# Optimization experiments

Hardware: AMD Instinct MI355X
Metric: run time of the kernel (lower is better)

Reference implementation:

```python
import jax, jax.numpy as jnp
import numpy as np

NUM_DIRECTIONS = 64
NUM_STEPS = 64
D = 64
NEG_INF = -1e9  # matches the original's -inf sentinel of 1e9


def _sample_directions(n):
    # Mirrors WeightedEulerCurve._obtainDirection with np.random.seed(4)
    np.random.seed(4)
    out = []
    for _ in range(n):
        phi = np.random.uniform(0, np.pi * 2)
        costheta = np.random.uniform(-1, 1)
        theta = np.arccos(costheta)
        out.append([np.sin(theta) * np.cos(phi), np.sin(theta) * np.sin(phi), np.cos(theta)])
    return np.asarray(out, dtype=np.float32)


def setup_inputs() -> dict:
    key = jax.random.key(0)
    # strictly positive -> dense cubical complex (every voxel is a vertex,
    # every adjacent pair an edge, etc.), matching torch.nonzero on x>0
    x = jax.random.uniform(key, (D, D, D), dtype=jnp.float32) + 1e-3
    dirs = jnp.asarray(_sample_directions(NUM_DIRECTIONS))  # (K, 3)
    return {"x": x, "dirs": dirs}


def _pairmax(a, axis):
    n = a.shape[axis]
    return jnp.maximum(jax.lax.slice_in_dim(a, 0, n - 1, axis=axis),
                       jax.lax.slice_in_dim(a, 1, n, axis=axis))


def _curve_contrib(heights, vals, intervals):
    # heights: (K, N) per-direction simplex heights; vals: (N,) shared weights
    K = heights.shape[0]
    idx = jnp.argsort(heights, axis=-1)
    sorted_h = jnp.take_along_axis(heights, idx, axis=-1)
    sorted_v = jnp.take(vals, idx)                                    # (K, N)
    csum = jnp.concatenate([jnp.zeros((K, 1), heights.dtype),
                            jnp.cumsum(sorted_v, axis=-1)], axis=-1)  # (K, N+1)
    padded_h = jnp.concatenate([jnp.full((K, 1), NEG_INF, heights.dtype),
                                sorted_h], axis=-1)                   # (K, N+1)
    ptr = jax.vmap(lambda h: jnp.searchsorted(h, intervals, side='right'))(padded_h) - 1
    return jnp.take_along_axis(csum, ptr, axis=-1)                    # (K, num_intervals)


def _wect(x, dirs, num_steps):
    d = x.shape[0]
    K = dirs.shape[0]
    r = jnp.arange(d, dtype=x.dtype)
    d0, d1, d2 = dirs[:, 0], dirs[:, 1], dirs[:, 2]
    # vertex heights per direction: H[k,i,j,l] = d0*i + d1*j + d2*l
    H = (d0[:, None, None, None] * r[:, None, None]
         + d1[:, None, None, None] * r[None, :, None]
         + d2[:, None, None, None] * r[None, None, :])
    p0, p1, p2 = (jax.nn.relu(d0)[:, None], jax.nn.relu(d1)[:, None], jax.nn.relu(d2)[:, None])

    min_h = -(3.0 ** 0.5) * d
    dh = (-2.0 * min_h) / num_steps
    intervals = jnp.asarray(min_h + dh * np.arange(num_steps + 1), dtype=x.dtype)

    # vertices
    vh = H.reshape(K, -1)
    vv = x.reshape(-1)

    # edges along each axis: max over the 2 endpoints -> base height + relu(d_axis)
    eh = jnp.concatenate([
        H[:, :-1].reshape(K, -1) + p0,
        H[:, :, :-1].reshape(K, -1) + p1,
        H[:, :, :, :-1].reshape(K, -1) + p2], axis=1)
    ev = jnp.concatenate([
        _pairmax(x, 0).reshape(-1),
        _pairmax(x, 1).reshape(-1),
        _pairmax(x, 2).reshape(-1)])

    # squares spanning axis pairs (1,2), (0,2), (0,1): max over 4 corners
    sh = jnp.concatenate([
        H[:, :, :-1, :-1].reshape(K, -1) + p1 + p2,
        H[:, :-1, :, :-1].reshape(K, -1) + p0 + p2,
        H[:, :-1, :-1, :].reshape(K, -1) + p0 + p1], axis=1)
    sv = jnp.concatenate([
        _pairmax(_pairmax(x, 1), 2).reshape(-1),
        _pairmax(_pairmax(x, 0), 2).reshape(-1),
        _pairmax(_pairmax(x, 0), 1).reshape(-1)])

    # cubes: max over 8 corners
    ch = H[:, :-1, :-1, :-1].reshape(K, -1) + p0 + p1 + p2
    cv = _pairmax(_pairmax(_pairmax(x, 0), 1), 2).reshape(-1)

    v = _curve_contrib(vh, vv, intervals)
    e = _curve_contrib(eh, ev, intervals)
    s = _curve_contrib(sh, sv, intervals)
    c = _curve_contrib(ch, cv, intervals)
    return v - e + s - c  # (K, num_steps + 1)


def reference(x, dirs):
    return _wect(x, dirs, NUM_STEPS)
```

## Files before the change

### kernel.cpp

```cpp
#include <hip/hip_runtime.h>
#include <math.h>

#define NDIRS 64
#define NBIN 65
#define HSTRIDE 66
#define HIST1 (NDIRS*HSTRIDE)
#define THREADS 256
#define WPB 4
#define SPW 2
#define NBLK 512
#define RROWS 64
#define ROWF (NDIRS*NBIN)

static constexpr float INV = 0.28867513459481287f;

__device__ __forceinline__ float rdlane(float v, int t) {
  return __int_as_float(__builtin_amdgcn_readlane(__float_as_int(v), t));
}

__global__ __launch_bounds__(THREADS) void wect_hist(
    const float* __restrict__ x, const float* __restrict__ dirs,
    float* __restrict__ accum) {
  __shared__ float hist[WPB * HIST1];
  const int tid = threadIdx.x;
  const int lane = tid & 63;
  const int wid  = tid >> 6;

  float4* h4 = (float4*)hist;
  for (int idx = tid; idx < WPB * HIST1 / 4; idx += THREADS)
    h4[idx] = make_float4(0.f, 0.f, 0.f, 0.f);
  __syncthreads();

  const float D0 = dirs[3*lane+0] * INV;
  const float D1 = dirs[3*lane+1] * INV;
  const float D2 = dirs[3*lane+2] * INV;
  const float Q1 = fmaxf(D0, 0.f);
  const float Q2 = fmaxf(D1, 0.f);
  const float Q3 = fmaxf(D2, 0.f);
  const float Q4 = Q2 + Q3;
  const float Q5 = Q1 + Q3;
  const float Q6 = Q1 + Q2;
  const float Q7 = Q1 + Q2 + Q3;

  float* __restrict__ myrow = hist + wid * HIST1 + lane * HSTRIDE;

  for (int s = 0; s < SPW; ++s) {
    const int strip = (blockIdx.x * WPB + wid) * SPW + s;
    const int i = strip >> 6, j = strip & 63;
    const int l = lane;
    const float* p = x + (strip << 6) + l;
    const int dL = (l < 63) ? 1 : 0;
    const int dJ = (j < 63) ? 64 : 0;
    const int dI = (i < 63) ? 4096 : 0;
    const bool iv = dI != 0, jv = dJ != 0, lv = dL != 0;

    const float x000 = p[0],       x001 = p[dL];
    const float x010 = p[dJ],      x011 = p[dJ+dL];
    const float x100 = p[dI],      x101 = p[dI+dL];
    const float x110 = p[dI+dJ],   x111 = p[dI+dJ+dL];

    const float e0m = fmaxf(x000, x100);
    const float e1m = fmaxf(x000, x010);
    const float e2m = fmaxf(x000, x001);
    const float s12 = fmaxf(fmaxf(e1m, x001), x011);
    const float s02 = fmaxf(fmaxf(e0m, x001), x101);
    const float s01 = fmaxf(fmaxf(e0m, x010), x110);
    const float cc  = fmaxf(fmaxf(s01, fmaxf(x001, x101)), fmaxf(x011, x111));

    const float v1 = iv ? -e0m : 0.f;
    const float v2 = jv ? -e1m : 0.f;
    const float v3 = lv ? -e2m : 0.f;
    const float v4 = (jv && lv) ? s12 : 0.f;
    const float v5 = (iv && lv) ? s02 : 0.f;
    const float v6 = (iv && jv) ? s01 : 0.f;
    const float v7 = (iv && jv && lv) ? -cc : 0.f;
    const float T  = x000 + v1+v2+v3+v4+v5+v6+v7;

    const float u0 = (float)i * D0 + (float)j * D1;

    #pragma unroll 8
    for (int t = 0; t < 64; ++t) {
      const float bT = rdlane(T,  t);
      const float b1 = rdlane(v1, t);
      const float b2 = rdlane(v2, t);
      const float b3 = rdlane(v3, t);
      const float b4 = rdlane(v4, t);
      const float b5 = rdlane(v5, t);
      const float b6 = rdlane(v6, t);
      const float b7 = rdlane(v7, t);
      const float u  = fmaf((float)t, D2, u0);
      const float bf = ceilf(u);
      const float fr = bf - u;
      const int   ib = (int)bf + 32;
      float S = 0.f;
      S += (Q1 > fr) ? b1 : 0.f;
      S += (Q2 > fr) ? b2 : 0.f;
      S += (Q3 > fr) ? b3 : 0.f;
      S += (Q4 > fr) ? b4 : 0.f;
      S += (Q5 > fr) ? b5 : 0.f;
      S += (Q6 > fr) ? b6 : 0.f;
      S += (Q7 > fr) ? b7 : 0.f;
      float* a = myrow + ib;
      const float r0 = a[0], r1 = a[1];
      a[0] = r0 + (bT - S);
      a[1] = r1 + S;
    }
  }

  __syncthreads();
  const int arow = (blockIdx.x & (RROWS - 1)) * ROWF;
  for (int z = tid; z < ROWF; z += THREADS) {
    const int r = z / NBIN, c = z - r * NBIN;
    const int li = r * HSTRIDE + c;
    const float sacc = hist[li] + hist[HIST1 + li]
                     + hist[2*HIST1 + li] + hist[3*HIST1 + li];
    unsafeAtomicAdd(&accum[arow + z], sacc);
  }
}

__global__ __launch_bounds__(128) void wect_scan(
    const float* __restrict__ accum, float* __restrict__ out) {
  __shared__ float s[NBIN];
  const int k = blockIdx.x, t = threadIdx.x;
  if (t < NBIN) {
    float v = 0.f;
    #pragma unroll
    for (int r = 0; r < RROWS; ++r) v += accum[r*ROWF + k*NBIN + t];
    s[t] = v;
  }
  __syncthreads();
  for (int off = 1; off < NBIN; off <<= 1) {
    float a = 0.f;
    if (t < NBIN && t >= off) a = s[t-off];
    __syncthreads();
    if (t < NBIN && t >= off) s[t] += a;
    __syncthreads();
  }
  if (t < NBIN) out[k*NBIN + t] = s[t];
}

extern "C" void kernel_launch(void* const* d_in, const int* in_sizes, int n_in,
                              void* d_out, int out_size, void* d_ws, size_t ws_size,
                              hipStream_t stream) {
  const float* x = (const float*)d_in[0];
  const float* dirs = (const float*)d_in[1];
  float* out = (float*)d_out;
  float* accum = (float*)d_ws;

  hipMemsetAsync(accum, 0, RROWS*ROWF*sizeof(float), stream);
  wect_hist<<<NBLK, THREADS, 0, stream>>>(x, dirs, accum);
  wect_scan<<<NDIRS, 128, 0, stream>>>(accum, out);
}
```

Measured before the change: 104.0 us.

## Stage per-voxel weights in LDS and write per-block partials instead of atomics

Replaces the eight readlane broadcasts per inner iteration with two float4 LDS loads from a per-wave staging buffer. Each block now stores its histogram to its own row of the workspace with plain stores, so the atomics and the memset are dropped. The scan kernel now reduces 512 partial rows instead of 64, which adds global read traffic in the second kernel.

```diff
diff --git a/kernel.cpp b/kernel.cpp
--- a/kernel.cpp
+++ b/kernel.cpp
@@ -5,23 +5,20 @@
 #define NBIN 65
 #define HSTRIDE 66
 #define HIST1 (NDIRS*HSTRIDE)
+#define STAGEF 512
 #define THREADS 256
 #define WPB 4
 #define SPW 2
 #define NBLK 512
-#define RROWS 64
 #define ROWF (NDIRS*NBIN)
 
 static constexpr float INV = 0.28867513459481287f;
-
-__device__ __forceinline__ float rdlane(float v, int t) {
-  return __int_as_float(__builtin_amdgcn_readlane(__float_as_int(v), t));
-}
 
 __global__ __launch_bounds__(THREADS) void wect_hist(
     const float* __restrict__ x, const float* __restrict__ dirs,
     float* __restrict__ accum) {
   __shared__ float hist[WPB * HIST1];
+  __shared__ float stage[WPB * STAGEF];
   const int tid = threadIdx.x;
   const int lane = tid & 63;
   const int wid  = tid >> 6;
@@ -43,6 +40,7 @@
   const float Q7 = Q1 + Q2 + Q3;
 
   float* __restrict__ myrow = hist + wid * HIST1 + lane * HSTRIDE;
+  float4* __restrict__ mystage = (float4*)(stage + wid * STAGEF);
 
   for (int s = 0; s < SPW; ++s) {
     const int strip = (blockIdx.x * WPB + wid) * SPW + s;
@@ -76,67 +74,71 @@
     const float v7 = (iv && jv && lv) ? -cc : 0.f;
     const float T  = x000 + v1+v2+v3+v4+v5+v6+v7;
 
+    mystage[2*lane]     = make_float4(T,  v1, v2, v3);
+    mystage[2*lane + 1] = make_float4(v4, v5, v6, v7);
+
     const float u0 = (float)i * D0 + (float)j * D1;
 
     #pragma unroll 8
     for (int t = 0; t < 64; ++t) {
-      const float bT = rdlane(T,  t);
-      const float b1 = rdlane(v1, t);
-      const float b2 = rdlane(v2, t);
-      const float b3 = rdlane(v3, t);
-      const float b4 = rdlane(v4, t);
-      const float b5 = rdlane(v5, t);
-      const float b6 = rdlane(v6, t);
-      const float b7 = rdlane(v7, t);
+      const float4 A = mystage[2*t];
+      const float4 B = mystage[2*t + 1];
       const float u  = fmaf((float)t, D2, u0);
       const float bf = ceilf(u);
       const float fr = bf - u;
       const int   ib = (int)bf + 32;
       float S = 0.f;
-      S += (Q1 > fr) ? b1 : 0.f;
-      S += (Q2 > fr) ? b2 : 0.f;
-      S += (Q3 > fr) ? b3 : 0.f;
-      S += (Q4 > fr) ? b4 : 0.f;
-      S += (Q5 > fr) ? b5 : 0.f;
-      S += (Q6 > fr) ? b6 : 0.f;
-      S += (Q7 > fr) ? b7 : 0.f;
+      S += (Q1 > fr) ? A.y : 0.f;
+      S += (Q2 > fr) ? A.z : 0.f;
+      S += (Q3 > fr) ? A.w : 0.f;
+      S += (Q4 > fr) ? B.x : 0.f;
+      S += (Q5 > fr) ? B.y : 0.f;
+      S += (Q6 > fr) ? B.z : 0.f;
+      S += (Q7 > fr) ? B.w : 0.f;
       float* a = myrow + ib;
       const float r0 = a[0], r1 = a[1];
-      a[0] = r0 + (bT - S);
+      a[0] = r0 + (A.x - S);
       a[1] = r1 + S;
     }
   }
 
   __syncthreads();
-  const int arow = (blockIdx.x & (RROWS - 1)) * ROWF;
+  float* __restrict__ obase = accum + blockIdx.x * ROWF;
   for (int z = tid; z < ROWF; z += THREADS) {
     const int r = z / NBIN, c = z - r * NBIN;
     const int li = r * HSTRIDE + c;
-    const float sacc = hist[li] + hist[HIST1 + li]
-                     + hist[2*HIST1 + li] + hist[3*HIST1 + li];
-    unsafeAtomicAdd(&accum[arow + z], sacc);
+    obase[z] = hist[li] + hist[HIST1 + li]
+             + hist[2*HIST1 + li] + hist[3*HIST1 + li];
   }
 }
 
-__global__ __launch_bounds__(128) void wect_scan(
+__global__ __launch_bounds__(512) void wect_scan(
     const float* __restrict__ accum, float* __restrict__ out) {
+  __shared__ float red[8 * NBIN];
   __shared__ float s[NBIN];
-  const int k = blockIdx.x, t = threadIdx.x;
-  if (t < NBIN) {
+  const int k = blockIdx.x, tid = threadIdx.x;
+  for (int z = tid; z < 8 * NBIN; z += 512) {
+    const int g = z / NBIN, c = z - g * NBIN;
+    float v = 0.f;
+    for (int r = g; r < NBLK; r += 8) v += accum[r * ROWF + k * NBIN + c];
+    red[z] = v;
+  }
+  __syncthreads();
+  if (tid < NBIN) {
     float v = 0.f;
     #pragma unroll
-    for (int r = 0; r < RROWS; ++r) v += accum[r*ROWF + k*NBIN + t];
-    s[t] = v;
+    for (int gg = 0; gg < 8; ++gg) v += red[gg * NBIN + tid];
+    s[tid] = v;
   }
   __syncthreads();
   for (int off = 1; off < NBIN; off <<= 1) {
     float a = 0.f;
-    if (t < NBIN && t >= off) a = s[t-off];
+    if (tid < NBIN && tid >= off) a = s[tid - off];
     __syncthreads();
-    if (t < NBIN && t >= off) s[t] += a;
+    if (tid < NBIN && tid >= off) s[tid] += a;
     __syncthreads();
   }
-  if (t < NBIN) out[k*NBIN + t] = s[t];
+  if (tid < NBIN) out[k * NBIN + tid] = s[tid];
 }
 
 extern "C" void kernel_launch(void* const* d_in, const int* in_sizes, int n_in,
@@ -147,7 +149,6 @@
   float* out = (float*)d_out;
   float* accum = (float*)d_ws;
 
-  hipMemsetAsync(accum, 0, RROWS*ROWF*sizeof(float), stream);
   wect_hist<<<NBLK, THREADS, 0, stream>>>(x, dirs, accum);
-  wect_scan<<<NDIRS, 128, 0, stream>>>(accum, out);
+  wect_scan<<<NDIRS, 512, 0, stream>>>(accum, out);
 }
```

After: 111.4 us. +7.1%, slower.

## Replace atomic histogram accumulation with per-block partial rows reduced in scan

Applied to the files above, without the earlier changes.

The histogram kernel now runs three waves per block over 683 blocks. Each block writes its own partial histogram row with plain stores instead of atomically adding into 64 shared rows, so the workspace memset launch is dropped. The scan kernel uses 512 threads to reduce all per-block partial rows in eight groups before the prefix scan. This removes atomic contention and one launch, but makes the workspace much larger and raises the memory traffic in the scan. The histogram row stride also shrinks from 66 to 65 floats to change the LDS bank mapping.

```diff
diff --git a/kernel.cpp b/kernel.cpp
--- a/kernel.cpp
+++ b/kernel.cpp
@@ -3,13 +3,12 @@
 
 #define NDIRS 64
 #define NBIN 65
-#define HSTRIDE 66
-#define HIST1 (NDIRS*HSTRIDE)
-#define THREADS 256
-#define WPB 4
-#define SPW 2
-#define NBLK 512
-#define RROWS 64
+#define HSTRIDE 65
+#define HIST1 4164
+#define THREADS 192
+#define WPB 3
+#define NBLK 683
+#define NPAIR 2048
 #define ROWF (NDIRS*NBIN)
 
 static constexpr float INV = 0.28867513459481287f;
@@ -44,99 +43,105 @@
 
   float* __restrict__ myrow = hist + wid * HIST1 + lane * HSTRIDE;
 
-  for (int s = 0; s < SPW; ++s) {
-    const int strip = (blockIdx.x * WPB + wid) * SPW + s;
-    const int i = strip >> 6, j = strip & 63;
-    const int l = lane;
-    const float* p = x + (strip << 6) + l;
-    const int dL = (l < 63) ? 1 : 0;
-    const int dJ = (j < 63) ? 64 : 0;
-    const int dI = (i < 63) ? 4096 : 0;
-    const bool iv = dI != 0, jv = dJ != 0, lv = dL != 0;
+  const int pm = blockIdx.x * WPB + wid;
+  if (pm < NPAIR) {
+    for (int s = 0; s < 2; ++s) {
+      const int strip = 2 * pm + s;
+      const int i = strip >> 6, j = strip & 63;
+      const int l = lane;
+      const float* p = x + (strip << 6) + l;
+      const int dL = (l < 63) ? 1 : 0;
+      const int dJ = (j < 63) ? 64 : 0;
+      const int dI = (i < 63) ? 4096 : 0;
+      const bool iv = dI != 0, jv = dJ != 0, lv = dL != 0;
 
-    const float x000 = p[0],       x001 = p[dL];
-    const float x010 = p[dJ],      x011 = p[dJ+dL];
-    const float x100 = p[dI],      x101 = p[dI+dL];
-    const float x110 = p[dI+dJ],   x111 = p[dI+dJ+dL];
+      const float x000 = p[0],       x001 = p[dL];
+      const float x010 = p[dJ],      x011 = p[dJ+dL];
+      const float x100 = p[dI],      x101 = p[dI+dL];
+      const float x110 = p[dI+dJ],   x111 = p[dI+dJ+dL];
 
-    const float e0m = fmaxf(x000, x100);
-    const float e1m = fmaxf(x000, x010);
-    const float e2m = fmaxf(x000, x001);
-    const float s12 = fmaxf(fmaxf(e1m, x001), x011);
-    const float s02 = fmaxf(fmaxf(e0m, x001), x101);
-    const float s01 = fmaxf(fmaxf(e0m, x010), x110);
-    const float cc  = fmaxf(fmaxf(s01, fmaxf(x001, x101)), fmaxf(x011, x111));
+      const float e0m = fmaxf(x000, x100);
+      const float e1m = fmaxf(x000, x010);
+      const float e2m = fmaxf(x000, x001);
+      const float s12 = fmaxf(fmaxf(e1m, x001), x011);
+      const float s02 = fmaxf(fmaxf(e0m, x001), x101);
+      const float s01 = fmaxf(fmaxf(e0m, x010), x110);
+      const float cc  = fmaxf(fmaxf(s01, fmaxf(x001, x101)), fmaxf(x011, x111));
 
-    const float v1 = iv ? -e0m : 0.f;
-    const float v2 = jv ? -e1m : 0.f;
-    const float v3 = lv ? -e2m : 0.f;
-    const float v4 = (jv && lv) ? s12 : 0.f;
-    const float v5 = (iv && lv) ? s02 : 0.f;
-    const float v6 = (iv && jv) ? s01 : 0.f;
-    const float v7 = (iv && jv && lv) ? -cc : 0.f;
-    const float T  = x000 + v1+v2+v3+v4+v5+v6+v7;
+      const float v1 = iv ? -e0m : 0.f;
+      const float v2 = jv ? -e1m : 0.f;
+      const float v3 = lv ? -e2m : 0.f;
+      const float v4 = (jv && lv) ? s12 : 0.f;
+      const float v5 = (iv && lv) ? s02 : 0.f;
+      const float v6 = (iv && jv) ? s01 : 0.f;
+      const float v7 = (iv && jv && lv) ? -cc : 0.f;
+      const float T  = x000 + v1+v2+v3+v4+v5+v6+v7;
 
-    const float u0 = (float)i * D0 + (float)j * D1;
+      const float u0 = (float)i * D0 + (float)j * D1;
 
-    #pragma unroll 8
-    for (int t = 0; t < 64; ++t) {
-      const float bT = rdlane(T,  t);
-      const float b1 = rdlane(v1, t);
-      const float b2 = rdlane(v2, t);
-      const float b3 = rdlane(v3, t);
-      const float b4 = rdlane(v4, t);
-      const float b5 = rdlane(v5, t);
-      const float b6 = rdlane(v6, t);
-      const float b7 = rdlane(v7, t);
-      const float u  = fmaf((float)t, D2, u0);
-      const float bf = ceilf(u);
-      const float fr = bf - u;
-      const int   ib = (int)bf + 32;
-      float S = 0.f;
-      S += (Q1 > fr) ? b1 : 0.f;
-      S += (Q2 > fr) ? b2 : 0.f;
-      S += (Q3 > fr) ? b3 : 0.f;
-      S += (Q4 > fr) ? b4 : 0.f;
-      S += (Q5 > fr) ? b5 : 0.f;
-      S += (Q6 > fr) ? b6 : 0.f;
-      S += (Q7 > fr) ? b7 : 0.f;
-      float* a = myrow + ib;
-      const float r0 = a[0], r1 = a[1];
-      a[0] = r0 + (bT - S);
-      a[1] = r1 + S;
+      #pragma unroll 8
+      for (int t = 0; t < 64; ++t) {
+        const float bT = rdlane(T,  t);
+        const float b1 = rdlane(v1, t);
+        const float b2 = rdlane(v2, t);
+        const float b3 = rdlane(v3, t);
+        const float b4 = rdlane(v4, t);
+        const float b5 = rdlane(v5, t);
+        const float b6 = rdlane(v6, t);
+        const float b7 = rdlane(v7, t);
+        const float u  = fmaf((float)t, D2, u0);
+        const float bf = ceilf(u);
+        const float fr = bf - u;
+        const int   ib = (int)bf + 32;
+        float S = 0.f;
+        S += (Q1 > fr) ? b1 : 0.f;
+        S += (Q2 > fr) ? b2 : 0.f;
+        S += (Q3 > fr) ? b3 : 0.f;
+        S += (Q4 > fr) ? b4 : 0.f;
+        S += (Q5 > fr) ? b5 : 0.f;
+        S += (Q6 > fr) ? b6 : 0.f;
+        S += (Q7 > fr) ? b7 : 0.f;
+        float* a = myrow + ib;
+        const float r0 = a[0], r1 = a[1];
+        a[0] = r0 + (bT - S);
+        a[1] = r1 + S;
+      }
     }
   }
 
   __syncthreads();
-  const int arow = (blockIdx.x & (RROWS - 1)) * ROWF;
-  for (int z = tid; z < ROWF; z += THREADS) {
-    const int r = z / NBIN, c = z - r * NBIN;
-    const int li = r * HSTRIDE + c;
-    const float sacc = hist[li] + hist[HIST1 + li]
-                     + hist[2*HIST1 + li] + hist[3*HIST1 + li];
-    unsafeAtomicAdd(&accum[arow + z], sacc);
-  }
+  float* __restrict__ obase = accum + blockIdx.x * ROWF;
+  for (int z = tid; z < ROWF; z += THREADS)
+    obase[z] = hist[z] + hist[HIST1 + z] + hist[2*HIST1 + z];
 }
 
-__global__ __launch_bounds__(128) void wect_scan(
+__global__ __launch_bounds__(512) void wect_scan(
     const float* __restrict__ accum, float* __restrict__ out) {
+  __shared__ float red[8 * NBIN];
   __shared__ float s[NBIN];
-  const int k = blockIdx.x, t = threadIdx.x;
-  if (t < NBIN) {
+  const int k = blockIdx.x, tid = threadIdx.x;
+  for (int z = tid; z < 8 * NBIN; z += 512) {
+    const int g = z / NBIN, c = z - g * NBIN;
+    float v = 0.f;
+    for (int r = g; r < NBLK; r += 8) v += accum[r * ROWF + k * NBIN + c];
+    red[z] = v;
+  }
+  __syncthreads();
+  if (tid < NBIN) {
     float v = 0.f;
     #pragma unroll
-    for (int r = 0; r < RROWS; ++r) v += accum[r*ROWF + k*NBIN + t];
-    s[t] = v;
+    for (int gg = 0; gg < 8; ++gg) v += red[gg * NBIN + tid];
+    s[tid] = v;
   }
   __syncthreads();
   for (int off = 1; off < NBIN; off <<= 1) {
     float a = 0.f;
-    if (t < NBIN && t >= off) a = s[t-off];
+    if (tid < NBIN && tid >= off) a = s[tid - off];
     __syncthreads();
-    if (t < NBIN && t >= off) s[t] += a;
+    if (tid < NBIN && tid >= off) s[tid] += a;
     __syncthreads();
   }
-  if (t < NBIN) out[k*NBIN + t] = s[t];
+  if (tid < NBIN) out[k * NBIN + tid] = s[tid];
 }
 
 extern "C" void kernel_launch(void* const* d_in, const int* in_sizes, int n_in,
@@ -147,7 +152,6 @@
   float* out = (float*)d_out;
   float* accum = (float*)d_ws;
 
-  hipMemsetAsync(accum, 0, RROWS*ROWF*sizeof(float), stream);
   wect_hist<<<NBLK, THREADS, 0, stream>>>(x, dirs, accum);
-  wect_scan<<<NDIRS, 128, 0, stream>>>(accum, out);
+  wect_scan<<<NDIRS, 512, 0, stream>>>(accum, out);
 }
```

Result: slower. 140.2 us (+34.8%).
